# Performance work log

Hardware: AMD Instinct MI355X
Metric: run time of the kernel (lower is better)

Reference implementation:

```python
import jax, jax.numpy as jnp
import numpy as np

EPS = 1e-16

def setup_inputs() -> dict:
    B, N, M, D = 32, 16384, 128, 1024
    L = 3 * M + 6  # write_lengths sum: k(M), beta(1), g(1), s(3), gamma(1), e(M), a(M)
    ks = jax.random.split(jax.random.key(0), 5)
    embeddings = jax.random.normal(ks[0], (B, D), jnp.float32)
    w_prev = jax.random.uniform(ks[1], (B, N), jnp.float32)
    w_prev = w_prev / jnp.sum(w_prev, axis=1, keepdims=True)  # valid address distribution
    mem = jax.random.normal(ks[2], (B, N, M), jnp.float32) * 0.05
    # Dense params: variance_scaling(1.4, fan_avg, uniform) ~ U(-lim, lim)
    lim = float(np.sqrt(3.0 * 1.4 / ((D + L) / 2.0)))
    W = jax.random.uniform(ks[3], (D, L), jnp.float32, -lim, lim)
    b = jax.random.normal(ks[4], (L,), jnp.float32) * 0.01
    return {"embeddings": embeddings, "w_prev": w_prev, "mem": mem, "W": W, "b": b}

def _forward(embeddings, w_prev, mem, W, b):
    M = mem.shape[-1]
    o = embeddings @ W + b  # [B, 3M+6]
    k = o[:, :M]
    beta = jax.nn.softplus(o[:, M:M + 1])
    g = jax.nn.sigmoid(o[:, M + 1:M + 2])
    s = jax.nn.softmax(o[:, M + 2:M + 5], axis=1)  # 3-tap shift
    gamma = 1.0 + jax.nn.softplus(o[:, M + 5:M + 6])
    e = jax.nn.sigmoid(o[:, M + 6:2 * M + 6])
    a = o[:, 2 * M + 6:]
    # content addressing: cosine similarity -> softmax(beta * sim)
    sim = jnp.einsum('bnm,bm->bn', mem, k) / (
        jnp.linalg.norm(mem, axis=-1) * jnp.linalg.norm(k, axis=-1, keepdims=True) + EPS)
    w_c = jax.nn.softmax(beta * sim, axis=1)
    # interpolation with previous weights
    w_g = g * w_c + (1.0 - g) * w_prev
    # circular convolution with 3-tap shift kernel s = [s(-1), s(0), s(+1)]
    w_t = (s[:, 0:1] * jnp.roll(w_g, 1, axis=1)
           + s[:, 1:2] * w_g
           + s[:, 2:3] * jnp.roll(w_g, -1, axis=1))
    # sharpening
    w_sh = w_t ** gamma
    w = w_sh / (jnp.sum(w_sh, axis=1, keepdims=True) + EPS)
    # erase + add write: mem' = mem * (1 - w e^T) + w a^T
    we = w[:, :, None] * e[:, None, :]  # [B, N, M]
    wa = w[:, :, None] * a[:, None, :]
    new_mem = mem * (1.0 - we) + wa
    return w, new_mem

def reference(embeddings, w_prev, mem, W, b):
    return _forward(embeddings, w_prev, mem, W, b)
```

## Files before the change

kernel.cpp:

```cpp
#include <hip/hip_runtime.h>
#include <math.h>

#define B 32
#define N 16384
#define M 128
#define D 1024
#define L 390
#define EPSF 1e-16f

#define O_OFF  0
#define S1_OFF (B*L)
#define S2_OFF (S1_OFF + B)
#define Z_OFF  (S2_OFF + B)

typedef float fvec4 __attribute__((ext_vector_type(4)));

__device__ __forceinline__ float softplusf(float x) {
    return x > 20.f ? x : log1pf(expf(x));
}
__device__ __forceinline__ float sigmoidf(float x) {
    return 1.f / (1.f + expf(-x));
}

__global__ __launch_bounds__(256) void k1_gemm(const float* __restrict__ emb,
                                               const float* __restrict__ W,
                                               const float* __restrict__ bias,
                                               float* __restrict__ ws) {
    __shared__ float embS[D];
    __shared__ float red[4][64];
    const int l0 = blockIdx.x * 64;
    const int b  = blockIdx.y;
    const int t  = threadIdx.x;
    for (int i = t; i < D; i += 256) embS[i] = emb[b * D + i];
    if (blockIdx.x == 0 && t == 0) {
        ws[S1_OFF + b] = 0.f;
        ws[S2_OFF + b] = 0.f;
    }
    __syncthreads();
    const int li = t & 63;
    const int q  = t >> 6;
    const int l  = l0 + li;
    float partial = 0.f;
    if (l < L) {
        const float* wp = W + (size_t)(q * 256) * L + l;
        #pragma unroll 8
        for (int d = 0; d < 256; ++d) partial += embS[q * 256 + d] * wp[(size_t)d * L];
    }
    red[q][li] = partial;
    __syncthreads();
    if (t < 64 && l0 + t < L) {
        float o = red[0][t] + red[1][t] + red[2][t] + red[3][t] + bias[l0 + t];
        ws[O_OFF + b * L + l0 + t] = o;
    }
}

__global__ __launch_bounds__(256) void k2_sim(const float* __restrict__ mem,
                                              float* __restrict__ ws) {
    const int b = blockIdx.y;
    const int t = threadIdx.x;
    const int n = blockIdx.x * 256 + t;
    const int wave = t >> 6, lane = t & 63;
    __shared__ float kS[M];
    __shared__ float par[2];
    __shared__ float acc[4];
    const float* o = ws + O_OFF + b * L;
    if (t < M) kS[t] = o[t];
    __syncthreads();
    if (t < M) {
        float kv = kS[t];
        float sq = kv * kv;
        #pragma unroll
        for (int off = 32; off >= 1; off >>= 1) sq += __shfl_xor(sq, off, 64);
        if (lane == 0) acc[t >> 6] = sq;
    }
    __syncthreads();
    if (t == 0) {
        par[0] = sqrtf(acc[0] + acc[1]);
        par[1] = softplusf(o[M]);
    }
    __syncthreads();
    const float knorm = par[0], beta = par[1];
    const float* mp = mem + ((size_t)b * N + n) * M;

    float dot = 0.f, sq = 0.f;
    #pragma unroll 16
    for (int j = 0; j < M / 4; ++j) {
        const fvec4 mv = *(const fvec4*)(mp + j * 4);
        const fvec4 kv = *(const fvec4*)&kS[j * 4];
        dot = fmaf(mv.x, kv.x, dot); dot = fmaf(mv.y, kv.y, dot);
        dot = fmaf(mv.z, kv.z, dot); dot = fmaf(mv.w, kv.w, dot);
        sq  = fmaf(mv.x, mv.x, sq);  sq  = fmaf(mv.y, mv.y, sq);
        sq  = fmaf(mv.z, mv.z, sq);  sq  = fmaf(mv.w, mv.w, sq);
    }
    const float sim = dot / (sqrtf(sq) * knorm + EPSF);
    const float uu  = expf(beta * sim);
    ws[Z_OFF + (size_t)b * N + n] = uu;

    float r = uu;
    #pragma unroll
    for (int off = 32; off >= 1; off >>= 1) r += __shfl_xor(r, off, 64);
    if (lane == 0) acc[wave] = r;
    __syncthreads();
    if (t == 0) atomicAdd(ws + S1_OFF + b, acc[0] + acc[1] + acc[2] + acc[3]);
}

__global__ __launch_bounds__(256) void k3_shsum(const float* __restrict__ w_prev,
                                                float* __restrict__ ws,
                                                float* __restrict__ out) {
    const int b = blockIdx.y;
    const int n = blockIdx.x * 256 + threadIdx.x;
    __shared__ float par[6];
    if (threadIdx.x == 0) {
        const float* o = ws + O_OFF + b * L;
        par[0] = sigmoidf(o[M + 1]);
        float x0 = o[M + 2], x1 = o[M + 3], x2 = o[M + 4];
        float mx = fmaxf(x0, fmaxf(x1, x2));
        float e0 = expf(x0 - mx), e1 = expf(x1 - mx), e2 = expf(x2 - mx);
        float inv = 1.f / (e0 + e1 + e2);
        par[1] = e0 * inv; par[2] = e1 * inv; par[3] = e2 * inv;
        par[4] = 1.f + softplusf(o[M + 5]);
        par[5] = 1.f / ws[S1_OFF + b];
    }
    __syncthreads();
    const float g = par[0], s0 = par[1], s1 = par[2], s2 = par[3];
    const float gamma = par[4], invS1 = par[5];
    const float* u  = ws + Z_OFF + (size_t)b * N;
    const float* wp = w_prev + (size_t)b * N;
    const int nm = (n == 0)     ? N - 1 : n - 1;
    const int np = (n == N - 1) ? 0     : n + 1;
    const float gm1 = 1.f - g;
    const float gi  = g * invS1;
    const float wgm = gi * u[nm] + gm1 * wp[nm];
    const float wg0 = gi * u[n ] + gm1 * wp[n ];
    const float wgp = gi * u[np] + gm1 * wp[np];
    const float wt  = s0 * wgm + s1 * wg0 + s2 * wgp;
    const float v = powf(wt, gamma);
    out[(size_t)b * N + n] = v;
    float r = v;
    #pragma unroll
    for (int off = 32; off >= 1; off >>= 1) r += __shfl_xor(r, off, 64);
    __shared__ float acc[4];
    if ((threadIdx.x & 63) == 0) acc[threadIdx.x >> 6] = r;
    __syncthreads();
    if (threadIdx.x == 0) atomicAdd(ws + S2_OFF + b, acc[0] + acc[1] + acc[2] + acc[3]);
}

__global__ __launch_bounds__(256) void k4_write(const float* __restrict__ mem,
                                                const float* __restrict__ ws,
                                                float* __restrict__ out) {
    const int b    = blockIdx.y;
    const int n0   = (gridDim.x - 1 - blockIdx.x) * 64;
    const int t    = threadIdx.x;
    const int wave = t >> 6, lane = t & 63;
    __shared__ float eS[M], aS[M];
    if (t < M) {
        eS[t] = sigmoidf(ws[O_OFF + b * L + M + 6 + t]);
        aS[t] = ws[O_OFF + b * L + 2 * M + 6 + t];
    }
    __syncthreads();
    const float invS2 = 1.f / (ws[S2_OFF + b] + EPSF);
    float* w_out = out + (size_t)b * N;
    float* m_out = out + (size_t)B * N;
    const int col  = (lane & 31) * 4;
    const int half = lane >> 5;
    const int base = n0 + wave * 16;
    const fvec4 ev = *(const fvec4*)&eS[col];
    const fvec4 av = *(const fvec4*)&aS[col];

    float wv[8];
    #pragma unroll
    for (int it = 0; it < 8; ++it)
        wv[it] = w_out[base + it * 2 + half] * invS2;

    #pragma unroll
    for (int it = 0; it < 8; ++it) {
        const int n = base + it * 2 + half;
        const size_t idx = ((size_t)b * N + n) * M + col;
        const fvec4 mv = *(const fvec4*)(mem + idx);
        const float w = wv[it];
        fvec4 r;
        r.x = fmaf(mv.x, fmaf(-w, ev.x, 1.f), w * av.x);
        r.y = fmaf(mv.y, fmaf(-w, ev.y, 1.f), w * av.y);
        r.z = fmaf(mv.z, fmaf(-w, ev.z, 1.f), w * av.z);
        r.w = fmaf(mv.w, fmaf(-w, ev.w, 1.f), w * av.w);
        __builtin_nontemporal_store(r, (fvec4*)(m_out + idx));
    }

    if ((lane & 31) == 0) {
        #pragma unroll
        for (int it = 0; it < 8; ++it)
            w_out[base + it * 2 + half] = wv[it];
    }
}

extern "C" void kernel_launch(void* const* d_in, const int* in_sizes, int n_in,
                              void* d_out, int out_size, void* d_ws, size_t ws_size,
                              hipStream_t stream) {
    const float* emb    = (const float*)d_in[0];
    const float* w_prev = (const float*)d_in[1];
    const float* mem    = (const float*)d_in[2];
    const float* W      = (const float*)d_in[3];
    const float* bias   = (const float*)d_in[4];
    float* ws  = (float*)d_ws;
    float* out = (float*)d_out;

    k1_gemm <<<dim3(7, B),       256, 0, stream>>>(emb, W, bias, ws);
    k2_sim  <<<dim3(N / 256, B), 256, 0, stream>>>(mem, ws);
    k3_shsum<<<dim3(N / 256, B), 256, 0, stream>>>(w_prev, ws, out);
    k4_write<<<dim3(N / 64, B),  256, 0, stream>>>(mem, ws, out);
}
```

Baseline: 537.7 us.

## Fuse sim, sharpen and write kernels into one cooperative persistent kernel

Merges the three per-batch kernels into a single cooperative kernel of 1024 blocks that uses grid-wide syncs between the similarity, shift/sharpen and memory-write phases. Each block handles a fixed contiguous chunk of one batch row in every phase, which removes two kernel launch boundaries and may improve L2 reuse of the mem chunk between the similarity read and the write pass. The cost is reduced parallelism (1024 blocks of 256 threads, capped by launch bounds) and the expense of the grid syncs. If the cooperative launch fails it falls back to the old kernels.

```diff
diff --git a/kernel.cpp b/kernel.cpp
--- a/kernel.cpp
+++ b/kernel.cpp
@@ -1,5 +1,8 @@
 #include <hip/hip_runtime.h>
+#include <hip/hip_cooperative_groups.h>
 #include <math.h>
+
+namespace cg = cooperative_groups;
 
 #define B 32
 #define N 16384
@@ -7,6 +10,10 @@
 #define D 1024
 #define L 390
 #define EPSF 1e-16f
+
+#define GRID  1024
+#define BPB   (GRID / B)
+#define CHUNK (N / BPB)
 
 #define O_OFF  0
 #define S1_OFF (B*L)
@@ -54,6 +61,149 @@
     }
 }
 
+__global__ __launch_bounds__(256, 4) void k234(const float* __restrict__ w_prev,
+                                               const float* __restrict__ mem,
+                                               float* __restrict__ ws,
+                                               float* __restrict__ out) {
+    cg::grid_group gg = cg::this_grid();
+    const int t    = threadIdx.x;
+    const int wave = t >> 6, lane = t & 63;
+    const int blk  = blockIdx.x;
+    const int b    = blk / BPB;
+    const int n0   = (blk % BPB) * CHUNK;
+    __shared__ float kS[M];
+    __shared__ float par[8];
+    __shared__ float acc[4];
+    const float* o = ws + O_OFF + b * L;
+
+    if (t < M) kS[t] = o[t];
+    __syncthreads();
+    if (t < M) {
+        float kv = kS[t];
+        float sq = kv * kv;
+        #pragma unroll
+        for (int off = 32; off >= 1; off >>= 1) sq += __shfl_xor(sq, off, 64);
+        if (lane == 0) acc[t >> 6] = sq;
+    }
+    __syncthreads();
+    if (t == 0) {
+        par[0] = sqrtf(acc[0] + acc[1]);
+        par[1] = softplusf(o[M]);
+    }
+    __syncthreads();
+    {
+        const float knorm = par[0], beta = par[1];
+        float s1sum = 0.f;
+        #pragma unroll
+        for (int h = 0; h < CHUNK / 256; ++h) {
+            const int n = n0 + h * 256 + t;
+            const float* mp = mem + ((size_t)b * N + n) * M;
+            float dot = 0.f, sq = 0.f;
+            #pragma unroll 16
+            for (int j = 0; j < M / 4; ++j) {
+                const fvec4 mv = *(const fvec4*)(mp + j * 4);
+                const fvec4 kv = *(const fvec4*)&kS[j * 4];
+                dot = fmaf(mv.x, kv.x, dot); dot = fmaf(mv.y, kv.y, dot);
+                dot = fmaf(mv.z, kv.z, dot); dot = fmaf(mv.w, kv.w, dot);
+                sq  = fmaf(mv.x, mv.x, sq);  sq  = fmaf(mv.y, mv.y, sq);
+                sq  = fmaf(mv.z, mv.z, sq);  sq  = fmaf(mv.w, mv.w, sq);
+            }
+            const float sim = dot / (sqrtf(sq) * knorm + EPSF);
+            const float uu  = expf(beta * sim);
+            ws[Z_OFF + (size_t)b * N + n] = uu;
+            s1sum += uu;
+        }
+        #pragma unroll
+        for (int off = 32; off >= 1; off >>= 1) s1sum += __shfl_xor(s1sum, off, 64);
+        if (lane == 0) acc[wave] = s1sum;
+        __syncthreads();
+        if (t == 0) atomicAdd(ws + S1_OFF + b, acc[0] + acc[1] + acc[2] + acc[3]);
+    }
+    gg.sync();
+
+    if (t == 0) {
+        par[2] = sigmoidf(o[M + 1]);
+        float x0 = o[M + 2], x1 = o[M + 3], x2 = o[M + 4];
+        float mx = fmaxf(x0, fmaxf(x1, x2));
+        float e0 = expf(x0 - mx), e1 = expf(x1 - mx), e2 = expf(x2 - mx);
+        float inv = 1.f / (e0 + e1 + e2);
+        par[3] = e0 * inv; par[4] = e1 * inv; par[5] = e2 * inv;
+        par[6] = 1.f + softplusf(o[M + 5]);
+        par[7] = 1.f / ws[S1_OFF + b];
+    }
+    __syncthreads();
+    {
+        const float g = par[2], s0 = par[3], s1v = par[4], s2v = par[5];
+        const float gamma = par[6], invS1 = par[7];
+        const float gm1 = 1.f - g, gi = g * invS1;
+        const float* u  = ws + Z_OFF + (size_t)b * N;
+        const float* wp = w_prev + (size_t)b * N;
+        float s2sum = 0.f;
+        #pragma unroll
+        for (int h = 0; h < CHUNK / 256; ++h) {
+            const int n  = n0 + h * 256 + t;
+            const int nm = (n == 0)     ? N - 1 : n - 1;
+            const int np = (n == N - 1) ? 0     : n + 1;
+            const float wgm = gi * u[nm] + gm1 * wp[nm];
+            const float wg0 = gi * u[n ] + gm1 * wp[n ];
+            const float wgp = gi * u[np] + gm1 * wp[np];
+            const float wt  = s0 * wgm + s1v * wg0 + s2v * wgp;
+            const float v = powf(wt, gamma);
+            out[(size_t)b * N + n] = v;
+            s2sum += v;
+        }
+        #pragma unroll
+        for (int off = 32; off >= 1; off >>= 1) s2sum += __shfl_xor(s2sum, off, 64);
+        __syncthreads();
+        if (lane == 0) acc[wave] = s2sum;
+        __syncthreads();
+        if (t == 0) atomicAdd(ws + S2_OFF + b, acc[0] + acc[1] + acc[2] + acc[3]);
+    }
+    gg.sync();
+
+    __shared__ float eS[M], aS[M];
+    if (t < M) {
+        eS[t] = sigmoidf(o[M + 6 + t]);
+        aS[t] = o[2 * M + 6 + t];
+    }
+    __syncthreads();
+    {
+        const float invS2 = 1.f / (ws[S2_OFF + b] + EPSF);
+        float* w_out = out + (size_t)b * N;
+        float* m_out = out + (size_t)B * N;
+        const int col  = (lane & 31) * 4;
+        const int half = lane >> 5;
+        const fvec4 ev = *(const fvec4*)&eS[col];
+        const fvec4 av = *(const fvec4*)&aS[col];
+        #pragma unroll
+        for (int tile = 0; tile < CHUNK / 64; ++tile) {
+            const int base = n0 + tile * 64 + wave * 16;
+            float wv[8];
+            #pragma unroll
+            for (int it = 0; it < 8; ++it)
+                wv[it] = w_out[base + it * 2 + half] * invS2;
+            #pragma unroll
+            for (int it = 0; it < 8; ++it) {
+                const int n = base + it * 2 + half;
+                const size_t idx = ((size_t)b * N + n) * M + col;
+                const fvec4 mv = *(const fvec4*)(mem + idx);
+                const float w = wv[it];
+                fvec4 r;
+                r.x = fmaf(mv.x, fmaf(-w, ev.x, 1.f), w * av.x);
+                r.y = fmaf(mv.y, fmaf(-w, ev.y, 1.f), w * av.y);
+                r.z = fmaf(mv.z, fmaf(-w, ev.z, 1.f), w * av.z);
+                r.w = fmaf(mv.w, fmaf(-w, ev.w, 1.f), w * av.w);
+                __builtin_nontemporal_store(r, (fvec4*)(m_out + idx));
+            }
+            if ((lane & 31) == 0) {
+                #pragma unroll
+                for (int it = 0; it < 8; ++it)
+                    w_out[base + it * 2 + half] = wv[it];
+            }
+        }
+    }
+}
+
 __global__ __launch_bounds__(256) void k2_sim(const float* __restrict__ mem,
                                               float* __restrict__ ws) {
     const int b = blockIdx.y;
@@ -81,7 +231,6 @@
     __syncthreads();
     const float knorm = par[0], beta = par[1];
     const float* mp = mem + ((size_t)b * N + n) * M;
-
     float dot = 0.f, sq = 0.f;
     #pragma unroll 16
     for (int j = 0; j < M / 4; ++j) {
@@ -95,7 +244,6 @@
     const float sim = dot / (sqrtf(sq) * knorm + EPSF);
     const float uu  = expf(beta * sim);
     ws[Z_OFF + (size_t)b * N + n] = uu;
-
     float r = uu;
     #pragma unroll
     for (int off = 32; off >= 1; off >>= 1) r += __shfl_xor(r, off, 64);
@@ -166,12 +314,10 @@
     const int base = n0 + wave * 16;
     const fvec4 ev = *(const fvec4*)&eS[col];
     const fvec4 av = *(const fvec4*)&aS[col];
-
     float wv[8];
     #pragma unroll
     for (int it = 0; it < 8; ++it)
         wv[it] = w_out[base + it * 2 + half] * invS2;
-
     #pragma unroll
     for (int it = 0; it < 8; ++it) {
         const int n = base + it * 2 + half;
@@ -185,7 +331,6 @@
         r.w = fmaf(mv.w, fmaf(-w, ev.w, 1.f), w * av.w);
         __builtin_nontemporal_store(r, (fvec4*)(m_out + idx));
     }
-
     if ((lane & 31) == 0) {
         #pragma unroll
         for (int it = 0; it < 8; ++it)
@@ -204,8 +349,15 @@
     float* ws  = (float*)d_ws;
     float* out = (float*)d_out;
 
-    k1_gemm <<<dim3(7, B),       256, 0, stream>>>(emb, W, bias, ws);
-    k2_sim  <<<dim3(N / 256, B), 256, 0, stream>>>(mem, ws);
-    k3_shsum<<<dim3(N / 256, B), 256, 0, stream>>>(w_prev, ws, out);
-    k4_write<<<dim3(N / 64, B),  256, 0, stream>>>(mem, ws, out);
-}
+    k1_gemm<<<dim3(7, B), 256, 0, stream>>>(emb, W, bias, ws);
+
+    void* args[] = {(void*)&w_prev, (void*)&mem, (void*)&ws, (void*)&out};
+    hipError_t err = hipLaunchCooperativeKernel((const void*)k234,
+                                                dim3(GRID), dim3(256),
+                                                args, 0, stream);
+    if (err != hipSuccess) {
+        k2_sim  <<<dim3(N / 256, B), 256, 0, stream>>>(mem, ws);
+        k3_shsum<<<dim3(N / 256, B), 256, 0, stream>>>(w_prev, ws, out);
+        k4_write<<<dim3(N / 64, B),  256, 0, stream>>>(mem, ws, out);
+    }
+}
```

After: 759.4 us. 41.2% more time.

## Coalesce similarity reads across lanes and recompute sharpened weights in write kernel

Applied to the files above, without the earlier changes.

The similarity kernel now assigns 16 lanes per memory row, with each lane loading 8 contiguous floats and the partial sums reduced by shuffles. This replaces the old one-row-per-thread strided loads with coalesced ones. The sharpening kernel no longer writes unnormalized weights to the output. The write kernel instead recomputes interpolation, shift and pow for its 64 rows, normalizes them, and shares them through LDS. This removes one global store and reload pass of the weight vector, at the cost of duplicated pow computation and an extra block barrier.

```diff
diff --git a/kernel.cpp b/kernel.cpp
--- a/kernel.cpp
+++ b/kernel.cpp
@@ -56,9 +56,9 @@
 
 __global__ __launch_bounds__(256) void k2_sim(const float* __restrict__ mem,
                                               float* __restrict__ ws) {
-    const int b = blockIdx.y;
-    const int t = threadIdx.x;
-    const int n = blockIdx.x * 256 + t;
+    const int b    = blockIdx.y;
+    const int n0   = blockIdx.x * 64;
+    const int t    = threadIdx.x;
     const int wave = t >> 6, lane = t & 63;
     __shared__ float kS[M];
     __shared__ float par[2];
@@ -80,33 +80,42 @@
     }
     __syncthreads();
     const float knorm = par[0], beta = par[1];
-    const float* mp = mem + ((size_t)b * N + n) * M;
-
-    float dot = 0.f, sq = 0.f;
-    #pragma unroll 16
-    for (int j = 0; j < M / 4; ++j) {
-        const fvec4 mv = *(const fvec4*)(mp + j * 4);
-        const fvec4 kv = *(const fvec4*)&kS[j * 4];
-        dot = fmaf(mv.x, kv.x, dot); dot = fmaf(mv.y, kv.y, dot);
-        dot = fmaf(mv.z, kv.z, dot); dot = fmaf(mv.w, kv.w, dot);
-        sq  = fmaf(mv.x, mv.x, sq);  sq  = fmaf(mv.y, mv.y, sq);
-        sq  = fmaf(mv.z, mv.z, sq);  sq  = fmaf(mv.w, mv.w, sq);
-    }
-    const float sim = dot / (sqrtf(sq) * knorm + EPSF);
-    const float uu  = expf(beta * sim);
-    ws[Z_OFF + (size_t)b * N + n] = uu;
-
-    float r = uu;
+    float* z = ws + Z_OFF + (size_t)b * N;
+    const int seg = (lane & 15) * 8;
+    const fvec4 ka = *(const fvec4*)&kS[seg];
+    const fvec4 kb = *(const fvec4*)&kS[seg + 4];
+    float lsum = 0.f;
     #pragma unroll
-    for (int off = 32; off >= 1; off >>= 1) r += __shfl_xor(r, off, 64);
-    if (lane == 0) acc[wave] = r;
+    for (int it = 0; it < 4; ++it) {
+        const int n = n0 + wave * 16 + it * 4 + (lane >> 4);
+        const float* mp = mem + ((size_t)b * N + n) * M + seg;
+        const fvec4 ma = *(const fvec4*)mp;
+        const fvec4 mb = *(const fvec4*)(mp + 4);
+        float dot = ma.x*ka.x + ma.y*ka.y + ma.z*ka.z + ma.w*ka.w
+                  + mb.x*kb.x + mb.y*kb.y + mb.z*kb.z + mb.w*kb.w;
+        float sq  = ma.x*ma.x + ma.y*ma.y + ma.z*ma.z + ma.w*ma.w
+                  + mb.x*mb.x + mb.y*mb.y + mb.z*mb.z + mb.w*mb.w;
+        #pragma unroll
+        for (int off = 1; off <= 8; off <<= 1) {
+            dot += __shfl_xor(dot, off, 64);
+            sq  += __shfl_xor(sq,  off, 64);
+        }
+        const float sim = dot / (sqrtf(sq) * knorm + EPSF);
+        const float uu  = expf(beta * sim);
+        if ((lane & 15) == 0) {
+            z[n] = uu;
+            lsum += uu;
+        }
+    }
+    lsum += __shfl_xor(lsum, 16, 64);
+    lsum += __shfl_xor(lsum, 32, 64);
+    if (lane == 0) acc[wave] = lsum;
     __syncthreads();
     if (t == 0) atomicAdd(ws + S1_OFF + b, acc[0] + acc[1] + acc[2] + acc[3]);
 }
 
-__global__ __launch_bounds__(256) void k3_shsum(const float* __restrict__ w_prev,
-                                                float* __restrict__ ws,
-                                                float* __restrict__ out) {
+__global__ __launch_bounds__(256) void k3_s2(const float* __restrict__ w_prev,
+                                             float* __restrict__ ws) {
     const int b = blockIdx.y;
     const int n = blockIdx.x * 256 + threadIdx.x;
     __shared__ float par[6];
@@ -135,7 +144,6 @@
     const float wgp = gi * u[np] + gm1 * wp[np];
     const float wt  = s0 * wgm + s1 * wg0 + s2 * wgp;
     const float v = powf(wt, gamma);
-    out[(size_t)b * N + n] = v;
     float r = v;
     #pragma unroll
     for (int off = 32; off >= 1; off >>= 1) r += __shfl_xor(r, off, 64);
@@ -146,50 +154,68 @@
 }
 
 __global__ __launch_bounds__(256) void k4_write(const float* __restrict__ mem,
+                                                const float* __restrict__ w_prev,
                                                 const float* __restrict__ ws,
                                                 float* __restrict__ out) {
     const int b    = blockIdx.y;
     const int n0   = (gridDim.x - 1 - blockIdx.x) * 64;
     const int t    = threadIdx.x;
     const int wave = t >> 6, lane = t & 63;
-    __shared__ float eS[M], aS[M];
+    __shared__ float eS[M], aS[M], wS[64];
+    __shared__ float par[8];
+    const float* o = ws + O_OFF + b * L;
     if (t < M) {
-        eS[t] = sigmoidf(ws[O_OFF + b * L + M + 6 + t]);
-        aS[t] = ws[O_OFF + b * L + 2 * M + 6 + t];
-    }
-    __syncthreads();
-    const float invS2 = 1.f / (ws[S2_OFF + b] + EPSF);
-    float* w_out = out + (size_t)b * N;
+        eS[t] = sigmoidf(o[M + 6 + t]);
+        aS[t] = o[2 * M + 6 + t];
+    }
+    if (t == 0) {
+        par[0] = sigmoidf(o[M + 1]);
+        float x0 = o[M + 2], x1 = o[M + 3], x2 = o[M + 4];
+        float mx = fmaxf(x0, fmaxf(x1, x2));
+        float e0 = expf(x0 - mx), e1 = expf(x1 - mx), e2 = expf(x2 - mx);
+        float inv = 1.f / (e0 + e1 + e2);
+        par[1] = e0 * inv; par[2] = e1 * inv; par[3] = e2 * inv;
+        par[4] = 1.f + softplusf(o[M + 5]);
+        par[5] = 1.f / ws[S1_OFF + b];
+        par[6] = 1.f / (ws[S2_OFF + b] + EPSF);
+    }
+    __syncthreads();
+    if (t < 64) {
+        const int n  = n0 + t;
+        const float g = par[0], s0 = par[1], s1v = par[2], s2v = par[3];
+        const float gamma = par[4], invS1 = par[5], invS2 = par[6];
+        const float gi = g * invS1, gm1 = 1.f - g;
+        const float* u  = ws + Z_OFF + (size_t)b * N;
+        const float* wp = w_prev + (size_t)b * N;
+        const int nm = (n == 0)     ? N - 1 : n - 1;
+        const int np = (n == N - 1) ? 0     : n + 1;
+        const float wgm = gi * u[nm] + gm1 * wp[nm];
+        const float wg0 = gi * u[n ] + gm1 * wp[n ];
+        const float wgp = gi * u[np] + gm1 * wp[np];
+        const float wt  = s0 * wgm + s1v * wg0 + s2v * wgp;
+        const float wv  = powf(wt, gamma) * invS2;
+        wS[t] = wv;
+        out[(size_t)b * N + n] = wv;
+    }
+    __syncthreads();
     float* m_out = out + (size_t)B * N;
     const int col  = (lane & 31) * 4;
     const int half = lane >> 5;
-    const int base = n0 + wave * 16;
     const fvec4 ev = *(const fvec4*)&eS[col];
     const fvec4 av = *(const fvec4*)&aS[col];
-
-    float wv[8];
-    #pragma unroll
-    for (int it = 0; it < 8; ++it)
-        wv[it] = w_out[base + it * 2 + half] * invS2;
-
     #pragma unroll
     for (int it = 0; it < 8; ++it) {
-        const int n = base + it * 2 + half;
+        const int loc = wave * 16 + it * 2 + half;
+        const int n   = n0 + loc;
+        const float w = wS[loc];
         const size_t idx = ((size_t)b * N + n) * M + col;
         const fvec4 mv = *(const fvec4*)(mem + idx);
-        const float w = wv[it];
         fvec4 r;
         r.x = fmaf(mv.x, fmaf(-w, ev.x, 1.f), w * av.x);
         r.y = fmaf(mv.y, fmaf(-w, ev.y, 1.f), w * av.y);
         r.z = fmaf(mv.z, fmaf(-w, ev.z, 1.f), w * av.z);
         r.w = fmaf(mv.w, fmaf(-w, ev.w, 1.f), w * av.w);
         __builtin_nontemporal_store(r, (fvec4*)(m_out + idx));
-    }
-
-    if ((lane & 31) == 0) {
-        #pragma unroll
-        for (int it = 0; it < 8; ++it)
-            w_out[base + it * 2 + half] = wv[it];
     }
 }
 
@@ -205,7 +231,7 @@
     float* out = (float*)d_out;
 
     k1_gemm <<<dim3(7, B),       256, 0, stream>>>(emb, W, bias, ws);
-    k2_sim  <<<dim3(N / 256, B), 256, 0, stream>>>(mem, ws);
-    k3_shsum<<<dim3(N / 256, B), 256, 0, stream>>>(w_prev, ws, out);
-    k4_write<<<dim3(N / 64, B),  256, 0, stream>>>(mem, ws, out);
-}
+    k2_sim  <<<dim3(N / 64, B),  256, 0, stream>>>(mem, ws);
+    k3_s2   <<<dim3(N / 256, B), 256, 0, stream>>>(w_prev, ws);
+    k4_write<<<dim3(N / 64, B),  256, 0, stream>>>(mem, w_prev, ws, out);
+}
```

After: 552.1 us. 1.03x slower.
